# Kernel optimization log

Hardware: AMD Instinct MI355X
Metric: run time of the kernel (lower is better)

## Reference

```python
import jax, jax.numpy as jnp
import numpy as np

B, S, D = 2, 2048, 2048
H = 16
Q_LORA, KV_LORA = 1536, 512
D_NOPE, D_ROPE, D_V = 128, 64, 128
D_QK = D_NOPE + D_ROPE  # 192
EPS = 1e-6


def rmsnorm(x, w):
    return x * jax.lax.rsqrt(jnp.mean(x * x, axis=-1, keepdims=True) + EPS) * w


def apply_rope(x, freqs_cis):
    # x: (B, S, h, D_ROPE); freqs_cis: (S, D_ROPE//2, 2) = (cos, sin)
    # DeepSeek pairs consecutive elements (2i, 2i+1) as complex re/im.
    b, s, h, d = x.shape
    xp = x.reshape(b, s, h, d // 2, 2)
    re, im = xp[..., 0], xp[..., 1]
    cos = freqs_cis[None, :, None, :, 0]
    sin = freqs_cis[None, :, None, :, 1]
    out_re = re * cos - im * sin
    out_im = re * sin + im * cos
    return jnp.stack([out_re, out_im], axis=-1).reshape(b, s, h, d)


def setup_inputs() -> dict:
    key = jax.random.key(0)
    ks = jax.random.split(key, 8)
    sd = 0.02
    x = jax.random.normal(ks[0], (B, S, D), dtype=jnp.float32)
    # RoPE table over the rope head dim
    inv_freq = 1.0 / (10000.0 ** (np.arange(0, D_ROPE, 2, dtype=np.float32) / D_ROPE))
    t = np.arange(S, dtype=np.float32)
    f = np.outer(t, inv_freq)  # (S, 32)
    freqs_cis = jnp.asarray(np.stack([np.cos(f), np.sin(f)], axis=-1), dtype=jnp.float32)
    return {
        "x": x,
        "start_pos": 0,
        "freqs_cis": freqs_cis,
        "wq_a": jax.random.normal(ks[1], (Q_LORA, D), dtype=jnp.float32) * sd,
        "q_norm_w": jnp.ones((Q_LORA,), dtype=jnp.float32),
        "wq_b": jax.random.normal(ks[2], (H * D_QK, Q_LORA), dtype=jnp.float32) * sd,
        "wkv_a": jax.random.normal(ks[3], (KV_LORA + D_ROPE, D), dtype=jnp.float32) * sd,
        "kv_norm_w": jnp.ones((KV_LORA,), dtype=jnp.float32),
        "wkv_b": jax.random.normal(ks[4], (H * (D_NOPE + D_V), KV_LORA), dtype=jnp.float32) * sd,
        "wo": jax.random.normal(ks[5], (D, H * D_V), dtype=jnp.float32) * sd,
    }


def reference(x, start_pos, freqs_cis, wq_a, q_norm_w, wq_b, wkv_a, kv_norm_w, wkv_b, wo):
    bsz, seqlen, _ = x.shape
    softmax_scale = D_QK ** (-0.5)

    # --- queries: low-rank down-proj, RMSNorm, up-proj ---
    q = rmsnorm(x @ wq_a.T, q_norm_w) @ wq_b.T          # (B,S,H*D_QK)
    q = q.reshape(bsz, seqlen, H, D_QK)
    q_nope, q_pe = q[..., :D_NOPE], q[..., D_NOPE:]
    q_pe = apply_rope(q_pe, freqs_cis)
    q = jnp.concatenate([q_nope, q_pe], axis=-1)         # (B,S,H,192)

    # --- keys/values: compressed latent + shared rope key ---
    kv = x @ wkv_a.T                                     # (B,S,KV_LORA+D_ROPE)
    kv_c, k_pe = kv[..., :KV_LORA], kv[..., KV_LORA:]
    k_pe = apply_rope(k_pe[:, :, None, :], freqs_cis)    # (B,S,1,64)
    kvb = rmsnorm(kv_c, kv_norm_w) @ wkv_b.T             # (B,S,H*(D_NOPE+D_V))
    kvb = kvb.reshape(bsz, seqlen, H, D_NOPE + D_V)
    k_nope, v = kvb[..., :D_NOPE], kvb[..., D_NOPE:]
    k = jnp.concatenate([k_nope, jnp.broadcast_to(k_pe, (bsz, seqlen, H, D_ROPE))], axis=-1)

    # --- causal attention (FA2 with attention_mask=None) ---
    scores = jnp.einsum("bqhd,bkhd->bhqk", q, k) * softmax_scale
    causal = jnp.tril(jnp.ones((seqlen, seqlen), dtype=bool))
    scores = jnp.where(causal[None, None], scores, jnp.finfo(scores.dtype).min)
    attn = jax.nn.softmax(scores, axis=-1)
    out = jnp.einsum("bhqk,bkhd->bqhd", attn, v)         # (B,S,H,D_V)
    # (v padding to qk_head_dim then slicing [..., :D_V] is a no-op)
    return out.reshape(bsz, seqlen, H * D_V) @ wo.T
```

## Files before the change

kernel.cpp:

```cpp
#include <hip/hip_runtime.h>
#include <math.h>

typedef short short8 __attribute__((ext_vector_type(8)));
typedef float float4v __attribute__((ext_vector_type(4)));
#define AS1 __attribute__((address_space(1)))
#define AS3 __attribute__((address_space(3)))

__device__ __forceinline__ float b2f(ushort u) {
    unsigned v = ((unsigned)u) << 16; float f; __builtin_memcpy(&f, &v, 4); return f;
}
__device__ __forceinline__ ushort f2b(float f) {
    unsigned v; __builtin_memcpy(&v, &f, 4);
    unsigned r = (v + 0x7fffu + ((v >> 16) & 1u)) >> 16;
    return (ushort)r;
}

__global__ void cvt_pad(const float* __restrict__ src, ushort* __restrict__ dst,
                        int src_rows, int cols, int total4) {
    int i = blockIdx.x * 256 + threadIdx.x;
    if (i >= total4) return;
    size_t e = (size_t)i * 4;
    int r = (int)(e / (size_t)cols);
    ushort4 o;
    if (r < src_rows) {
        float4 v = *(const float4*)(src + e);
        o.x = f2b(v.x); o.y = f2b(v.y); o.z = f2b(v.z); o.w = f2b(v.w);
    } else {
        o.x = 0; o.y = 0; o.z = 0; o.w = 0;
    }
    *(ushort4*)(dst + e) = o;
}

__global__ __launch_bounds__(256)
void gemm_bt(const ushort* __restrict__ A, const ushort* __restrict__ B,
             void* __restrict__ Cv, int K, int ldc, int nstore, int f32out) {
    __shared__ ushort sA[128 * 32];
    __shared__ ushort sB[128 * 32];
    const int tid = threadIdx.x;
    const int wave = tid >> 6, lane = tid & 63;
    const int bm = blockIdx.y * 128, bn = blockIdx.x * 128;
    const int wm = (wave >> 1) * 64, wn = (wave & 1) * 64;
    float4v acc[4][4] = {};

    const int srow = wave * 32 + (lane >> 2);
    const int skc = (lane & 3) * 8;
    const ushort* Ag = A + (size_t)(bm + srow) * K + skc;
    const ushort* Bg = B + (size_t)(bn + srow) * K + skc;
    ushort* sAw = sA + (wave * 32) * 32;
    ushort* sBw = sB + (wave * 32) * 32;

    for (int k0 = 0; k0 < K; k0 += 32) {
        __builtin_amdgcn_global_load_lds((const AS1 void*)(Ag + k0), (AS3 void*)sAw, 16, 0, 0);
        __builtin_amdgcn_global_load_lds((const AS1 void*)(Ag + (size_t)16 * K + k0),
                                         (AS3 void*)(sAw + 16 * 32), 16, 0, 0);
        __builtin_amdgcn_global_load_lds((const AS1 void*)(Bg + k0), (AS3 void*)sBw, 16, 0, 0);
        __builtin_amdgcn_global_load_lds((const AS1 void*)(Bg + (size_t)16 * K + k0),
                                         (AS3 void*)(sBw + 16 * 32), 16, 0, 0);
        __syncthreads();
        short8 af[4], bfr[4];
#pragma unroll
        for (int i = 0; i < 4; ++i) {
            af[i]  = *(const short8*)(sA + (wm + i * 16 + (lane & 15)) * 32 + (lane >> 4) * 8);
            bfr[i] = *(const short8*)(sB + (wn + i * 16 + (lane & 15)) * 32 + (lane >> 4) * 8);
        }
#pragma unroll
        for (int i = 0; i < 4; ++i)
#pragma unroll
            for (int j = 0; j < 4; ++j)
                acc[i][j] = __builtin_amdgcn_mfma_f32_16x16x32_bf16(af[i], bfr[j], acc[i][j], 0, 0, 0);
        __syncthreads();
    }
#pragma unroll
    for (int i = 0; i < 4; ++i) {
        int row0 = bm + wm + i * 16 + (lane >> 4) * 4;
#pragma unroll
        for (int j = 0; j < 4; ++j) {
            int col = bn + wn + j * 16 + (lane & 15);
            if (col < nstore) {
                if (f32out) {
                    float* C = (float*)Cv;
#pragma unroll
                    for (int r = 0; r < 4; ++r)
                        C[(size_t)(row0 + r) * ldc + col] = acc[i][j][r];
                } else {
                    ushort* C = (ushort*)Cv;
#pragma unroll
                    for (int r = 0; r < 4; ++r)
                        C[(size_t)(row0 + r) * ldc + col] = f2b(acc[i][j][r]);
                }
            }
        }
    }
}

__global__ void rmsnorm_inplace(ushort* __restrict__ d, const float* __restrict__ w, int cols) {
    int row = blockIdx.x, tid = threadIdx.x;
    ushort* p = d + (size_t)row * cols;
    float ss = 0.f;
    for (int i = tid; i < cols; i += 256) { float v = b2f(p[i]); ss += v * v; }
#pragma unroll
    for (int off = 32; off >= 1; off >>= 1) ss += __shfl_xor(ss, off);
    __shared__ float red[4];
    if ((tid & 63) == 0) red[tid >> 6] = ss;
    __syncthreads();
    float tot = red[0] + red[1] + red[2] + red[3];
    float rs = rsqrtf(tot / (float)cols + 1e-6f);
    for (int i = tid; i < cols; i += 256) p[i] = f2b(b2f(p[i]) * rs * w[i]);
}

__global__ void kvnorm_rope(const ushort* __restrict__ kvraw, const float* __restrict__ w,
                            const float* __restrict__ freqs, ushort* __restrict__ kvc,
                            ushort* __restrict__ kpe) {
    int row = blockIdx.x, tid = threadIdx.x;
    int s = row & 2047;
    const ushort* p = kvraw + (size_t)row * 576;
    float v0 = b2f(p[tid]), v1 = b2f(p[tid + 256]);
    float ss = v0 * v0 + v1 * v1;
#pragma unroll
    for (int off = 32; off >= 1; off >>= 1) ss += __shfl_xor(ss, off);
    __shared__ float red[4];
    if ((tid & 63) == 0) red[tid >> 6] = ss;
    __syncthreads();
    float tot = red[0] + red[1] + red[2] + red[3];
    float rs = rsqrtf(tot / 512.f + 1e-6f);
    kvc[(size_t)row * 512 + tid] = f2b(v0 * rs * w[tid]);
    kvc[(size_t)row * 512 + tid + 256] = f2b(v1 * rs * w[tid + 256]);
    if (tid < 32) {
        float re = b2f(p[512 + 2 * tid]), im = b2f(p[512 + 2 * tid + 1]);
        float cs = freqs[(s * 32 + tid) * 2], sn = freqs[(s * 32 + tid) * 2 + 1];
        kpe[(size_t)row * 64 + 2 * tid] = f2b(re * cs - im * sn);
        kpe[(size_t)row * 64 + 2 * tid + 1] = f2b(re * sn + im * cs);
    }
}

__global__ void qrope(ushort* __restrict__ q, const float* __restrict__ freqs) {
    int idx = blockIdx.x * 256 + threadIdx.x;
    int i = idx & 31;
    int h = (idx >> 5) & 15;
    int srow = idx >> 9;
    int s = srow & 2047;
    ushort* p = q + ((size_t)srow * 16 + h) * 192 + 128 + 2 * i;
    float re = b2f(p[0]), im = b2f(p[1]);
    float cs = freqs[(s * 32 + i) * 2], sn = freqs[(s * 32 + i) * 2 + 1];
    p[0] = f2b(re * cs - im * sn);
    p[1] = f2b(re * sn + im * cs);
}

__global__ void k_repack(const ushort* __restrict__ kvb, const ushort* __restrict__ kpe,
                         ushort* __restrict__ Kfull) {
    int tid = threadIdx.x;
    int row = blockIdx.x * 8 + (tid >> 5);
    int c = tid & 31;
    int bh = row >> 11, s = row & 2047;
    int b = bh >> 4, h = bh & 15;
    size_t sg = (size_t)b * 2048 + s;
    short8 v = {0, 0, 0, 0, 0, 0, 0, 0};
    if (c < 16)      v = *(const short8*)(kvb + sg * 4096 + h * 256 + c * 8);
    else if (c < 24) v = *(const short8*)(kpe + sg * 64 + (c - 16) * 8);
    if (c < 25) *(short8*)(Kfull + (size_t)row * 200 + c * 8) = v;
}

__global__ __launch_bounds__(256)
void v_repack(const ushort* __restrict__ kvb, ushort* __restrict__ Vt) {
    __shared__ ushort sT[64][136];
    int tid = threadIdx.x;
    int kt = blockIdx.x, bh = blockIdx.y;
    int b = bh >> 4, h = bh & 15;
#pragma unroll
    for (int k = 0; k < 4; ++k) {
        int id = k * 256 + tid;
        int r = id >> 4, c8 = id & 15;
        size_t sg = (size_t)b * 2048 + kt * 64 + r;
        *(short8*)(&sT[r][c8 * 8]) = *(const short8*)(kvb + sg * 4096 + h * 256 + 128 + c8 * 8);
    }
    __syncthreads();
    int d = tid >> 1, half = tid & 1;
    ushort tmp[32];
#pragma unroll
    for (int i = 0; i < 32; ++i) tmp[i] = sT[half * 32 + i][d];
    ushort* dst = Vt + (((size_t)bh * 32 + kt) * 128 + d) * 72 + half * 32;
#pragma unroll
    for (int i = 0; i < 4; ++i) *(short8*)(dst + i * 8) = *(const short8*)(tmp + i * 8);
}

__global__ __launch_bounds__(256)
void mla_attn2(const ushort* __restrict__ q, const ushort* __restrict__ Kfull,
               const ushort* __restrict__ Vt, ushort* __restrict__ out, float scale) {
    __shared__ ushort sK[64 * 200];
    __shared__ ushort sV[128 * 72];
    __shared__ ushort sP[4][16][72];
    const int tid = threadIdx.x, wave = tid >> 6, lane = tid & 63;
    const int p = blockIdx.x, bh = blockIdx.y;
    const int b = bh >> 4, h = bh & 15;
    const ushort* Kb = Kfull + (size_t)bh * 2048 * 200;
    const ushort* Vb = Vt + (size_t)bh * 32 * 128 * 72;

    for (int phase = 0; phase < 2; ++phase) {
        const int qt = (phase == 0) ? (31 - p) : p;
        const int qrow = qt * 64 + wave * 16 + (lane & 15);
        const ushort* qp = q + ((size_t)(b * 2048 + qrow) * 16 + h) * 192 + (lane >> 4) * 8;
        short8 qf[6];
#pragma unroll
        for (int c = 0; c < 6; ++c) qf[c] = *(const short8*)(qp + c * 32);

        float4v oacc[8] = {};
        float m_i[4] = {-INFINITY, -INFINITY, -INFINITY, -INFINITY};
        float l_i[4] = {0.f, 0.f, 0.f, 0.f};
        const int myrow0 = qt * 64 + wave * 16 + (lane >> 4) * 4;

        for (int kt = 0; kt <= qt; ++kt) {
            const ushort* Ksrc = Kb + (size_t)kt * 64 * 200;
            const ushort* Vsrc = Vb + (size_t)kt * 128 * 72;
#pragma unroll
            for (int i = 0; i < 7; ++i) {
                int s0 = i * 256 + wave * 64;
                if (s0 < 1600)
                    __builtin_amdgcn_global_load_lds(
                        (const AS1 void*)(Ksrc + (size_t)(s0 + lane) * 8),
                        (AS3 void*)(sK + s0 * 8), 16, 0, 0);
            }
#pragma unroll
            for (int i = 0; i < 5; ++i) {
                int s0 = i * 256 + wave * 64;
                if (s0 < 1152)
                    __builtin_amdgcn_global_load_lds(
                        (const AS1 void*)(Vsrc + (size_t)(s0 + lane) * 8),
                        (AS3 void*)(sV + s0 * 8), 16, 0, 0);
            }
            __syncthreads();
            float4v sc[4];
#pragma unroll
            for (int ct = 0; ct < 4; ++ct) {
                float4v a = {0.f, 0.f, 0.f, 0.f};
#pragma unroll
                for (int c = 0; c < 6; ++c) {
                    short8 kf = *(const short8*)(sK + (ct * 16 + (lane & 15)) * 200 + c * 32 + (lane >> 4) * 8);
                    a = __builtin_amdgcn_mfma_f32_16x16x32_bf16(qf[c], kf, a, 0, 0, 0);
                }
                sc[ct] = a;
            }
            float mnew[4];
#pragma unroll
            for (int r = 0; r < 4; ++r) mnew[r] = m_i[r];
#pragma unroll
            for (int ct = 0; ct < 4; ++ct)
#pragma unroll
                for (int r = 0; r < 4; ++r) {
                    float v = sc[ct][r] * scale;
                    if (kt == qt && (kt * 64 + ct * 16 + (lane & 15)) > (myrow0 + r)) v = -INFINITY;
                    sc[ct][r] = v;
                    mnew[r] = fmaxf(mnew[r], v);
                }
#pragma unroll
            for (int off = 8; off >= 1; off >>= 1)
#pragma unroll
                for (int r = 0; r < 4; ++r) mnew[r] = fmaxf(mnew[r], __shfl_xor(mnew[r], off));
            float alpha[4], psum[4];
#pragma unroll
            for (int r = 0; r < 4; ++r) {
                alpha[r] = __expf(m_i[r] - mnew[r]);
                m_i[r] = mnew[r];
                psum[r] = 0.f;
            }
#pragma unroll
            for (int ct = 0; ct < 4; ++ct)
#pragma unroll
                for (int r = 0; r < 4; ++r) {
                    float pv = __expf(sc[ct][r] - mnew[r]);
                    psum[r] += pv;
                    sP[wave][(lane >> 4) * 4 + r][ct * 16 + (lane & 15)] = f2b(pv);
                }
#pragma unroll
            for (int off = 8; off >= 1; off >>= 1)
#pragma unroll
                for (int r = 0; r < 4; ++r) psum[r] += __shfl_xor(psum[r], off);
#pragma unroll
            for (int r = 0; r < 4; ++r) l_i[r] = l_i[r] * alpha[r] + psum[r];
#pragma unroll
            for (int dt = 0; dt < 8; ++dt)
#pragma unroll
                for (int r = 0; r < 4; ++r) oacc[dt][r] *= alpha[r];
            __syncthreads();
#pragma unroll
            for (int kc = 0; kc < 2; ++kc) {
                short8 pf = *(const short8*)(&sP[wave][lane & 15][kc * 32 + (lane >> 4) * 8]);
#pragma unroll
                for (int dt = 0; dt < 8; ++dt) {
                    short8 vf = *(const short8*)(sV + (dt * 16 + (lane & 15)) * 72 + kc * 32 + (lane >> 4) * 8);
                    oacc[dt] = __builtin_amdgcn_mfma_f32_16x16x32_bf16(pf, vf, oacc[dt], 0, 0, 0);
                }
            }
            __syncthreads();
        }
#pragma unroll
        for (int dt = 0; dt < 8; ++dt) {
#pragma unroll
            for (int r = 0; r < 4; ++r) {
                int row = myrow0 + r;
                out[((size_t)(b * 2048 + row) * 16 + h) * 128 + dt * 16 + (lane & 15)] =
                    f2b(oacc[dt][r] / l_i[r]);
            }
        }
    }
}

extern "C" void kernel_launch(void* const* d_in, const int* in_sizes, int n_in,
                              void* d_out, int out_size, void* d_ws, size_t ws_size,
                              hipStream_t stream) {
    const float* x     = (const float*)d_in[0];
    const float* freqs = (const float*)d_in[2];
    const float* wq_a  = (const float*)d_in[3];
    const float* qnw   = (const float*)d_in[4];
    const float* wq_b  = (const float*)d_in[5];
    const float* wkv_a = (const float*)d_in[6];
    const float* kvnw  = (const float*)d_in[7];
    const float* wkv_b = (const float*)d_in[8];
    const float* wo    = (const float*)d_in[9];

    char* ws = (char*)d_ws;
    size_t off = 0;
    auto alloc = [&](size_t n) { char* p = ws + off; off += (n + 255) & ~(size_t)255; return p; };
    ushort* xb    = (ushort*)alloc(4096ull * 2048 * 2);
    ushort* wqab  = (ushort*)alloc(1536ull * 2048 * 2);
    ushort* wqbb  = (ushort*)alloc(3072ull * 1536 * 2);
    ushort* wkvab = (ushort*)alloc(640ull * 2048 * 2);
    ushort* wkvbb = (ushort*)alloc(4096ull * 512 * 2);
    ushort* wob   = (ushort*)alloc(2048ull * 2048 * 2);
    ushort* qa    = (ushort*)alloc(4096ull * 1536 * 2);
    ushort* kvraw = (ushort*)alloc(4096ull * 576 * 2);
    ushort* kvc   = (ushort*)alloc(4096ull * 512 * 2);
    ushort* kpe   = (ushort*)alloc(4096ull * 64 * 2);
    ushort* qfull = (ushort*)alloc(4096ull * 3072 * 2);
    ushort* kvbuf = (ushort*)alloc(4096ull * 4096 * 2);
    ushort* attno = (ushort*)alloc(4096ull * 2048 * 2);
    if (off > ws_size) return;
    ushort* Kfull = (ushort*)xb;
    ushort* Vt = (ushort*)qa;

    auto cvt = [&](const float* s, ushort* dd, int sr, int cols, size_t dtot) {
        int t4 = (int)(dtot / 4);
        cvt_pad<<<(t4 + 255) / 256, 256, 0, stream>>>(s, dd, sr, cols, t4);
    };
    cvt(x, xb, 4096, 2048, 4096ull * 2048);
    cvt(wq_a, wqab, 1536, 2048, 1536ull * 2048);
    cvt(wq_b, wqbb, 3072, 1536, 3072ull * 1536);
    cvt(wkv_a, wkvab, 576, 2048, 640ull * 2048);
    cvt(wkv_b, wkvbb, 4096, 512, 4096ull * 512);
    cvt(wo, wob, 2048, 2048, 2048ull * 2048);

    gemm_bt<<<dim3(12, 32), 256, 0, stream>>>(xb, wqab, qa, 2048, 1536, 1536, 0);
    gemm_bt<<<dim3(5, 32), 256, 0, stream>>>(xb, wkvab, kvraw, 2048, 576, 576, 0);
    rmsnorm_inplace<<<4096, 256, 0, stream>>>(qa, qnw, 1536);
    kvnorm_rope<<<4096, 256, 0, stream>>>(kvraw, kvnw, freqs, kvc, kpe);
    gemm_bt<<<dim3(24, 32), 256, 0, stream>>>(qa, wqbb, qfull, 1536, 3072, 3072, 0);
    qrope<<<8192, 256, 0, stream>>>(qfull, freqs);
    gemm_bt<<<dim3(32, 32), 256, 0, stream>>>(kvc, wkvbb, kvbuf, 512, 4096, 4096, 0);
    k_repack<<<8192, 256, 0, stream>>>(kvbuf, kpe, Kfull);
    v_repack<<<dim3(32, 32), 256, 0, stream>>>(kvbuf, Vt);
    const float scale = 1.0f / sqrtf(192.0f);
    mla_attn2<<<dim3(16, 32), 256, 0, stream>>>(qfull, Kfull, Vt, attno, scale);
    gemm_bt<<<dim3(16, 32), 256, 0, stream>>>(attno, wob, (float*)d_out, 2048, 2048, 2048, 1);
}
```

Before: 550.2 us.

## Fuse q/kv down-projection GEMMs and rework attention to keep P in registers

The two down-projection weight matrices are packed into one buffer, so a single GEMM produces the q latent and the kv latent into a shared strided buffer. The norm and GEMM kernels gain leading-dimension arguments to read from it. The attention kernel now computes S^T (K as the A operand), so each lane owns one query row. This lets softmax stats reduce across only two shuffles and P feed the PV MFMA straight from registers, removing the LDS round trip and a barrier. The grid changes from 16 paired-phase blocks to 32 single-tile blocks, and the PV product uses 16x16x16 MFMAs, which issue more, smaller instructions.

```diff
diff --git a/kernel.cpp b/kernel.cpp
--- a/kernel.cpp
+++ b/kernel.cpp
@@ -2,6 +2,7 @@
 #include <math.h>
 
 typedef short short8 __attribute__((ext_vector_type(8)));
+typedef short short4v __attribute__((ext_vector_type(4)));
 typedef float float4v __attribute__((ext_vector_type(4)));
 #define AS1 __attribute__((address_space(1)))
 #define AS3 __attribute__((address_space(3)))
@@ -13,6 +14,18 @@
     unsigned v; __builtin_memcpy(&v, &f, 4);
     unsigned r = (v + 0x7fffu + ((v >> 16) & 1u)) >> 16;
     return (ushort)r;
+}
+
+__device__ __forceinline__ float4v pv_mfma(short4v a, short4v b, float4v c) {
+#if __has_builtin(__builtin_amdgcn_mfma_f32_16x16x16_bf16)
+    return __builtin_amdgcn_mfma_f32_16x16x16_bf16(a, b, c, 0, 0, 0);
+#elif __has_builtin(__builtin_amdgcn_mfma_f32_16x16x16bf16_1k)
+    return __builtin_amdgcn_mfma_f32_16x16x16bf16_1k(a, b, c, 0, 0, 0);
+#else
+    short8 a8 = {a[0], a[1], a[2], a[3], 0, 0, 0, 0};
+    short8 b8 = {b[0], b[1], b[2], b[3], 0, 0, 0, 0};
+    return __builtin_amdgcn_mfma_f32_16x16x32_bf16(a8, b8, c, 0, 0, 0);
+#endif
 }
 
 __global__ void cvt_pad(const float* __restrict__ src, ushort* __restrict__ dst,
@@ -33,7 +46,7 @@
 
 __global__ __launch_bounds__(256)
 void gemm_bt(const ushort* __restrict__ A, const ushort* __restrict__ B,
-             void* __restrict__ Cv, int K, int ldc, int nstore, int f32out) {
+             void* __restrict__ Cv, int K, int lda, int ldb, int ldc, int f32out) {
     __shared__ ushort sA[128 * 32];
     __shared__ ushort sB[128 * 32];
     const int tid = threadIdx.x;
@@ -44,17 +57,17 @@
 
     const int srow = wave * 32 + (lane >> 2);
     const int skc = (lane & 3) * 8;
-    const ushort* Ag = A + (size_t)(bm + srow) * K + skc;
-    const ushort* Bg = B + (size_t)(bn + srow) * K + skc;
+    const ushort* Ag = A + (size_t)(bm + srow) * lda + skc;
+    const ushort* Bg = B + (size_t)(bn + srow) * ldb + skc;
     ushort* sAw = sA + (wave * 32) * 32;
     ushort* sBw = sB + (wave * 32) * 32;
 
     for (int k0 = 0; k0 < K; k0 += 32) {
         __builtin_amdgcn_global_load_lds((const AS1 void*)(Ag + k0), (AS3 void*)sAw, 16, 0, 0);
-        __builtin_amdgcn_global_load_lds((const AS1 void*)(Ag + (size_t)16 * K + k0),
+        __builtin_amdgcn_global_load_lds((const AS1 void*)(Ag + (size_t)16 * lda + k0),
                                          (AS3 void*)(sAw + 16 * 32), 16, 0, 0);
         __builtin_amdgcn_global_load_lds((const AS1 void*)(Bg + k0), (AS3 void*)sBw, 16, 0, 0);
-        __builtin_amdgcn_global_load_lds((const AS1 void*)(Bg + (size_t)16 * K + k0),
+        __builtin_amdgcn_global_load_lds((const AS1 void*)(Bg + (size_t)16 * ldb + k0),
                                          (AS3 void*)(sBw + 16 * 32), 16, 0, 0);
         __syncthreads();
         short8 af[4], bfr[4];
@@ -76,26 +89,25 @@
 #pragma unroll
         for (int j = 0; j < 4; ++j) {
             int col = bn + wn + j * 16 + (lane & 15);
-            if (col < nstore) {
-                if (f32out) {
-                    float* C = (float*)Cv;
-#pragma unroll
-                    for (int r = 0; r < 4; ++r)
-                        C[(size_t)(row0 + r) * ldc + col] = acc[i][j][r];
-                } else {
-                    ushort* C = (ushort*)Cv;
-#pragma unroll
-                    for (int r = 0; r < 4; ++r)
-                        C[(size_t)(row0 + r) * ldc + col] = f2b(acc[i][j][r]);
-                }
-            }
-        }
-    }
-}
-
-__global__ void rmsnorm_inplace(ushort* __restrict__ d, const float* __restrict__ w, int cols) {
+            if (f32out) {
+                float* C = (float*)Cv;
+#pragma unroll
+                for (int r = 0; r < 4; ++r)
+                    C[(size_t)(row0 + r) * ldc + col] = acc[i][j][r];
+            } else {
+                ushort* C = (ushort*)Cv;
+#pragma unroll
+                for (int r = 0; r < 4; ++r)
+                    C[(size_t)(row0 + r) * ldc + col] = f2b(acc[i][j][r]);
+            }
+        }
+    }
+}
+
+__global__ void rmsnorm_inplace(ushort* __restrict__ d, const float* __restrict__ w,
+                                int cols, int ld) {
     int row = blockIdx.x, tid = threadIdx.x;
-    ushort* p = d + (size_t)row * cols;
+    ushort* p = d + (size_t)row * ld;
     float ss = 0.f;
     for (int i = tid; i < cols; i += 256) { float v = b2f(p[i]); ss += v * v; }
 #pragma unroll
@@ -110,10 +122,10 @@
 
 __global__ void kvnorm_rope(const ushort* __restrict__ kvraw, const float* __restrict__ w,
                             const float* __restrict__ freqs, ushort* __restrict__ kvc,
-                            ushort* __restrict__ kpe) {
+                            ushort* __restrict__ kpe, int ld) {
     int row = blockIdx.x, tid = threadIdx.x;
     int s = row & 2047;
-    const ushort* p = kvraw + (size_t)row * 576;
+    const ushort* p = kvraw + (size_t)row * ld;
     float v0 = b2f(p[tid]), v1 = b2f(p[tid + 256]);
     float ss = v0 * v0 + v1 * v1;
 #pragma unroll
@@ -184,123 +196,106 @@
 }
 
 __global__ __launch_bounds__(256)
-void mla_attn2(const ushort* __restrict__ q, const ushort* __restrict__ Kfull,
+void mla_attn3(const ushort* __restrict__ q, const ushort* __restrict__ Kfull,
                const ushort* __restrict__ Vt, ushort* __restrict__ out, float scale) {
     __shared__ ushort sK[64 * 200];
     __shared__ ushort sV[128 * 72];
-    __shared__ ushort sP[4][16][72];
     const int tid = threadIdx.x, wave = tid >> 6, lane = tid & 63;
-    const int p = blockIdx.x, bh = blockIdx.y;
+    const int lq = lane & 15, quad = lane >> 4;
+    const int qt = 31 - blockIdx.x;
+    const int bh = blockIdx.y;
     const int b = bh >> 4, h = bh & 15;
     const ushort* Kb = Kfull + (size_t)bh * 2048 * 200;
     const ushort* Vb = Vt + (size_t)bh * 32 * 128 * 72;
 
-    for (int phase = 0; phase < 2; ++phase) {
-        const int qt = (phase == 0) ? (31 - p) : p;
-        const int qrow = qt * 64 + wave * 16 + (lane & 15);
-        const ushort* qp = q + ((size_t)(b * 2048 + qrow) * 16 + h) * 192 + (lane >> 4) * 8;
-        short8 qf[6];
-#pragma unroll
-        for (int c = 0; c < 6; ++c) qf[c] = *(const short8*)(qp + c * 32);
-
-        float4v oacc[8] = {};
-        float m_i[4] = {-INFINITY, -INFINITY, -INFINITY, -INFINITY};
-        float l_i[4] = {0.f, 0.f, 0.f, 0.f};
-        const int myrow0 = qt * 64 + wave * 16 + (lane >> 4) * 4;
-
-        for (int kt = 0; kt <= qt; ++kt) {
-            const ushort* Ksrc = Kb + (size_t)kt * 64 * 200;
-            const ushort* Vsrc = Vb + (size_t)kt * 128 * 72;
-#pragma unroll
-            for (int i = 0; i < 7; ++i) {
-                int s0 = i * 256 + wave * 64;
-                if (s0 < 1600)
-                    __builtin_amdgcn_global_load_lds(
-                        (const AS1 void*)(Ksrc + (size_t)(s0 + lane) * 8),
-                        (AS3 void*)(sK + s0 * 8), 16, 0, 0);
-            }
-#pragma unroll
-            for (int i = 0; i < 5; ++i) {
-                int s0 = i * 256 + wave * 64;
-                if (s0 < 1152)
-                    __builtin_amdgcn_global_load_lds(
-                        (const AS1 void*)(Vsrc + (size_t)(s0 + lane) * 8),
-                        (AS3 void*)(sV + s0 * 8), 16, 0, 0);
-            }
-            __syncthreads();
-            float4v sc[4];
+    const int q_abs = qt * 64 + wave * 16 + lq;
+    const ushort* qp = q + ((size_t)(b * 2048 + q_abs) * 16 + h) * 192 + quad * 8;
+    short8 qf[6];
+#pragma unroll
+    for (int c = 0; c < 6; ++c) qf[c] = *(const short8*)(qp + c * 32);
+
+    float4v oacc[8] = {};
+    float m_i = -INFINITY, l_i = 0.f;
+
+    for (int kt = 0; kt <= qt; ++kt) {
+        const ushort* Ksrc = Kb + (size_t)kt * 64 * 200;
+        const ushort* Vsrc = Vb + (size_t)kt * 128 * 72;
+#pragma unroll
+        for (int i = 0; i < 7; ++i) {
+            int s0 = i * 256 + wave * 64;
+            if (s0 < 1600)
+                __builtin_amdgcn_global_load_lds((const AS1 void*)(Ksrc + (size_t)(s0 + lane) * 8),
+                                                 (AS3 void*)(sK + s0 * 8), 16, 0, 0);
+        }
+#pragma unroll
+        for (int i = 0; i < 5; ++i) {
+            int s0 = i * 256 + wave * 64;
+            if (s0 < 1152)
+                __builtin_amdgcn_global_load_lds((const AS1 void*)(Vsrc + (size_t)(s0 + lane) * 8),
+                                                 (AS3 void*)(sV + s0 * 8), 16, 0, 0);
+        }
+        __syncthreads();
+        float4v sc[4];
+#pragma unroll
+        for (int ct = 0; ct < 4; ++ct) {
+            float4v a = {0.f, 0.f, 0.f, 0.f};
+#pragma unroll
+            for (int c = 0; c < 6; ++c) {
+                short8 kf = *(const short8*)(sK + (ct * 16 + lq) * 200 + c * 32 + quad * 8);
+                a = __builtin_amdgcn_mfma_f32_16x16x32_bf16(kf, qf[c], a, 0, 0, 0);
+            }
+            sc[ct] = a;
+        }
+        float mx = m_i;
+#pragma unroll
+        for (int ct = 0; ct < 4; ++ct)
+#pragma unroll
+            for (int r = 0; r < 4; ++r) {
+                float v = sc[ct][r] * scale;
+                int kv = kt * 64 + ct * 16 + quad * 4 + r;
+                if (kv > q_abs) v = -INFINITY;
+                sc[ct][r] = v;
+                mx = fmaxf(mx, v);
+            }
+        mx = fmaxf(mx, __shfl_xor(mx, 16));
+        mx = fmaxf(mx, __shfl_xor(mx, 32));
+        float alpha = __expf(m_i - mx);
+        m_i = mx;
+        float ps = 0.f;
+        short4v pf[4];
+#pragma unroll
+        for (int ct = 0; ct < 4; ++ct)
+#pragma unroll
+            for (int r = 0; r < 4; ++r) {
+                float pv = __expf(sc[ct][r] - mx);
+                ps += pv;
+                pf[ct][r] = (short)f2b(pv);
+            }
+        ps += __shfl_xor(ps, 16);
+        ps += __shfl_xor(ps, 32);
+        l_i = l_i * alpha + ps;
+#pragma unroll
+        for (int dt = 0; dt < 8; ++dt)
+#pragma unroll
+            for (int r = 0; r < 4; ++r) oacc[dt][r] *= alpha;
+#pragma unroll
+        for (int dt = 0; dt < 8; ++dt)
 #pragma unroll
             for (int ct = 0; ct < 4; ++ct) {
-                float4v a = {0.f, 0.f, 0.f, 0.f};
-#pragma unroll
-                for (int c = 0; c < 6; ++c) {
-                    short8 kf = *(const short8*)(sK + (ct * 16 + (lane & 15)) * 200 + c * 32 + (lane >> 4) * 8);
-                    a = __builtin_amdgcn_mfma_f32_16x16x32_bf16(qf[c], kf, a, 0, 0, 0);
-                }
-                sc[ct] = a;
-            }
-            float mnew[4];
-#pragma unroll
-            for (int r = 0; r < 4; ++r) mnew[r] = m_i[r];
-#pragma unroll
-            for (int ct = 0; ct < 4; ++ct)
-#pragma unroll
-                for (int r = 0; r < 4; ++r) {
-                    float v = sc[ct][r] * scale;
-                    if (kt == qt && (kt * 64 + ct * 16 + (lane & 15)) > (myrow0 + r)) v = -INFINITY;
-                    sc[ct][r] = v;
-                    mnew[r] = fmaxf(mnew[r], v);
-                }
-#pragma unroll
-            for (int off = 8; off >= 1; off >>= 1)
-#pragma unroll
-                for (int r = 0; r < 4; ++r) mnew[r] = fmaxf(mnew[r], __shfl_xor(mnew[r], off));
-            float alpha[4], psum[4];
-#pragma unroll
-            for (int r = 0; r < 4; ++r) {
-                alpha[r] = __expf(m_i[r] - mnew[r]);
-                m_i[r] = mnew[r];
-                psum[r] = 0.f;
-            }
-#pragma unroll
-            for (int ct = 0; ct < 4; ++ct)
-#pragma unroll
-                for (int r = 0; r < 4; ++r) {
-                    float pv = __expf(sc[ct][r] - mnew[r]);
-                    psum[r] += pv;
-                    sP[wave][(lane >> 4) * 4 + r][ct * 16 + (lane & 15)] = f2b(pv);
-                }
-#pragma unroll
-            for (int off = 8; off >= 1; off >>= 1)
-#pragma unroll
-                for (int r = 0; r < 4; ++r) psum[r] += __shfl_xor(psum[r], off);
-#pragma unroll
-            for (int r = 0; r < 4; ++r) l_i[r] = l_i[r] * alpha[r] + psum[r];
-#pragma unroll
-            for (int dt = 0; dt < 8; ++dt)
-#pragma unroll
-                for (int r = 0; r < 4; ++r) oacc[dt][r] *= alpha[r];
-            __syncthreads();
-#pragma unroll
-            for (int kc = 0; kc < 2; ++kc) {
-                short8 pf = *(const short8*)(&sP[wave][lane & 15][kc * 32 + (lane >> 4) * 8]);
-#pragma unroll
-                for (int dt = 0; dt < 8; ++dt) {
-                    short8 vf = *(const short8*)(sV + (dt * 16 + (lane & 15)) * 72 + kc * 32 + (lane >> 4) * 8);
-                    oacc[dt] = __builtin_amdgcn_mfma_f32_16x16x32_bf16(pf, vf, oacc[dt], 0, 0, 0);
-                }
-            }
-            __syncthreads();
-        }
-#pragma unroll
-        for (int dt = 0; dt < 8; ++dt) {
-#pragma unroll
-            for (int r = 0; r < 4; ++r) {
-                int row = myrow0 + r;
-                out[((size_t)(b * 2048 + row) * 16 + h) * 128 + dt * 16 + (lane & 15)] =
-                    f2b(oacc[dt][r] / l_i[r]);
-            }
-        }
+                short4v vf = *(const short4v*)(sV + (dt * 16 + lq) * 72 + ct * 16 + quad * 4);
+                oacc[dt] = pv_mfma(vf, pf[ct], oacc[dt]);
+            }
+        __syncthreads();
+    }
+    float inv = 1.f / l_i;
+#pragma unroll
+    for (int dt = 0; dt < 8; ++dt) {
+        ushort4 o;
+        o.x = f2b(oacc[dt][0] * inv);
+        o.y = f2b(oacc[dt][1] * inv);
+        o.z = f2b(oacc[dt][2] * inv);
+        o.w = f2b(oacc[dt][3] * inv);
+        *(ushort4*)(out + ((size_t)(b * 2048 + q_abs) * 16 + h) * 128 + dt * 16 + quad * 4) = o;
     }
 }
 
@@ -321,13 +316,11 @@
     size_t off = 0;
     auto alloc = [&](size_t n) { char* p = ws + off; off += (n + 255) & ~(size_t)255; return p; };
     ushort* xb    = (ushort*)alloc(4096ull * 2048 * 2);
-    ushort* wqab  = (ushort*)alloc(1536ull * 2048 * 2);
+    ushort* wqkva = (ushort*)alloc(2176ull * 2048 * 2);
     ushort* wqbb  = (ushort*)alloc(3072ull * 1536 * 2);
-    ushort* wkvab = (ushort*)alloc(640ull * 2048 * 2);
     ushort* wkvbb = (ushort*)alloc(4096ull * 512 * 2);
     ushort* wob   = (ushort*)alloc(2048ull * 2048 * 2);
-    ushort* qa    = (ushort*)alloc(4096ull * 1536 * 2);
-    ushort* kvraw = (ushort*)alloc(4096ull * 576 * 2);
+    ushort* qakv  = (ushort*)alloc(4096ull * 2176 * 2);
     ushort* kvc   = (ushort*)alloc(4096ull * 512 * 2);
     ushort* kpe   = (ushort*)alloc(4096ull * 64 * 2);
     ushort* qfull = (ushort*)alloc(4096ull * 3072 * 2);
@@ -335,29 +328,28 @@
     ushort* attno = (ushort*)alloc(4096ull * 2048 * 2);
     if (off > ws_size) return;
     ushort* Kfull = (ushort*)xb;
-    ushort* Vt = (ushort*)qa;
+    ushort* Vt = (ushort*)qakv;
 
     auto cvt = [&](const float* s, ushort* dd, int sr, int cols, size_t dtot) {
         int t4 = (int)(dtot / 4);
         cvt_pad<<<(t4 + 255) / 256, 256, 0, stream>>>(s, dd, sr, cols, t4);
     };
     cvt(x, xb, 4096, 2048, 4096ull * 2048);
-    cvt(wq_a, wqab, 1536, 2048, 1536ull * 2048);
+    cvt(wq_a, wqkva, 1536, 2048, 1536ull * 2048);
+    cvt(wkv_a, wqkva + 1536ull * 2048, 576, 2048, 640ull * 2048);
     cvt(wq_b, wqbb, 3072, 1536, 3072ull * 1536);
-    cvt(wkv_a, wkvab, 576, 2048, 640ull * 2048);
     cvt(wkv_b, wkvbb, 4096, 512, 4096ull * 512);
     cvt(wo, wob, 2048, 2048, 2048ull * 2048);
 
-    gemm_bt<<<dim3(12, 32), 256, 0, stream>>>(xb, wqab, qa, 2048, 1536, 1536, 0);
-    gemm_bt<<<dim3(5, 32), 256, 0, stream>>>(xb, wkvab, kvraw, 2048, 576, 576, 0);
-    rmsnorm_inplace<<<4096, 256, 0, stream>>>(qa, qnw, 1536);
-    kvnorm_rope<<<4096, 256, 0, stream>>>(kvraw, kvnw, freqs, kvc, kpe);
-    gemm_bt<<<dim3(24, 32), 256, 0, stream>>>(qa, wqbb, qfull, 1536, 3072, 3072, 0);
+    gemm_bt<<<dim3(17, 32), 256, 0, stream>>>(xb, wqkva, qakv, 2048, 2048, 2048, 2176, 0);
+    rmsnorm_inplace<<<4096, 256, 0, stream>>>(qakv, qnw, 1536, 2176);
+    kvnorm_rope<<<4096, 256, 0, stream>>>(qakv + 1536, kvnw, freqs, kvc, kpe, 2176);
+    gemm_bt<<<dim3(24, 32), 256, 0, stream>>>(qakv, wqbb, qfull, 1536, 2176, 1536, 3072, 0);
     qrope<<<8192, 256, 0, stream>>>(qfull, freqs);
-    gemm_bt<<<dim3(32, 32), 256, 0, stream>>>(kvc, wkvbb, kvbuf, 512, 4096, 4096, 0);
+    gemm_bt<<<dim3(32, 32), 256, 0, stream>>>(kvc, wkvbb, kvbuf, 512, 512, 512, 4096, 0);
     k_repack<<<8192, 256, 0, stream>>>(kvbuf, kpe, Kfull);
     v_repack<<<dim3(32, 32), 256, 0, stream>>>(kvbuf, Vt);
     const float scale = 1.0f / sqrtf(192.0f);
-    mla_attn2<<<dim3(16, 32), 256, 0, stream>>>(qfull, Kfull, Vt, attno, scale);
-    gemm_bt<<<dim3(16, 32), 256, 0, stream>>>(attno, wob, (float*)d_out, 2048, 2048, 2048, 1);
-}
+    mla_attn3<<<dim3(32, 32), 256, 0, stream>>>(qfull, Kfull, Vt, attno, scale);
+    gemm_bt<<<dim3(16, 32), 256, 0, stream>>>(attno, wob, (float*)d_out, 2048, 2048, 2048, 2048, 1);
+}
```

After: 561.3 us. 2.0% more time.

## Merge q/kv down-projections and fuse K/V repacking into up-projection epilogue

Applied to the files above, without the earlier changes.

The q and kv down-projection weights are concatenated so a single GEMM computes both, and the norm kernels read them through a row stride. The kv up-projection GEMM gains a scatter epilogue that writes K-nope straight into the padded K layout and V transposed into the attention tile layout, which removes the k_repack and v_repack kernels and the intermediate kvbuf round trip. A small kernel fills the rope part of K. The attention kernel also drops one barrier before the PV step, since each wave only reads its own P slice, and replaces the per-element divide with a multiply by a reciprocal. The V epilogue writes scattered 8-byte stores, which may coalesce poorly.

```diff
diff --git a/kernel.cpp b/kernel.cpp
--- a/kernel.cpp
+++ b/kernel.cpp
@@ -33,35 +33,37 @@
 
 __global__ __launch_bounds__(256)
 void gemm_bt(const ushort* __restrict__ A, const ushort* __restrict__ B,
-             void* __restrict__ Cv, int K, int ldc, int nstore, int f32out) {
+             void* __restrict__ Cv, int K, int lda, int ldb, int ldc, int mode,
+             ushort* __restrict__ Kf, ushort* __restrict__ Vtp) {
     __shared__ ushort sA[128 * 32];
     __shared__ ushort sB[128 * 32];
     const int tid = threadIdx.x;
     const int wave = tid >> 6, lane = tid & 63;
     const int bm = blockIdx.y * 128, bn = blockIdx.x * 128;
     const int wm = (wave >> 1) * 64, wn = (wave & 1) * 64;
+    const int lq = lane & 15, quad = lane >> 4;
     float4v acc[4][4] = {};
 
     const int srow = wave * 32 + (lane >> 2);
     const int skc = (lane & 3) * 8;
-    const ushort* Ag = A + (size_t)(bm + srow) * K + skc;
-    const ushort* Bg = B + (size_t)(bn + srow) * K + skc;
+    const ushort* Ag = A + (size_t)(bm + srow) * lda + skc;
+    const ushort* Bg = B + (size_t)(bn + srow) * ldb + skc;
     ushort* sAw = sA + (wave * 32) * 32;
     ushort* sBw = sB + (wave * 32) * 32;
 
     for (int k0 = 0; k0 < K; k0 += 32) {
         __builtin_amdgcn_global_load_lds((const AS1 void*)(Ag + k0), (AS3 void*)sAw, 16, 0, 0);
-        __builtin_amdgcn_global_load_lds((const AS1 void*)(Ag + (size_t)16 * K + k0),
+        __builtin_amdgcn_global_load_lds((const AS1 void*)(Ag + (size_t)16 * lda + k0),
                                          (AS3 void*)(sAw + 16 * 32), 16, 0, 0);
         __builtin_amdgcn_global_load_lds((const AS1 void*)(Bg + k0), (AS3 void*)sBw, 16, 0, 0);
-        __builtin_amdgcn_global_load_lds((const AS1 void*)(Bg + (size_t)16 * K + k0),
+        __builtin_amdgcn_global_load_lds((const AS1 void*)(Bg + (size_t)16 * ldb + k0),
                                          (AS3 void*)(sBw + 16 * 32), 16, 0, 0);
         __syncthreads();
         short8 af[4], bfr[4];
 #pragma unroll
         for (int i = 0; i < 4; ++i) {
-            af[i]  = *(const short8*)(sA + (wm + i * 16 + (lane & 15)) * 32 + (lane >> 4) * 8);
-            bfr[i] = *(const short8*)(sB + (wn + i * 16 + (lane & 15)) * 32 + (lane >> 4) * 8);
+            af[i]  = *(const short8*)(sA + (wm + i * 16 + lq) * 32 + quad * 8);
+            bfr[i] = *(const short8*)(sB + (wn + i * 16 + lq) * 32 + quad * 8);
         }
 #pragma unroll
         for (int i = 0; i < 4; ++i)
@@ -72,30 +74,46 @@
     }
 #pragma unroll
     for (int i = 0; i < 4; ++i) {
-        int row0 = bm + wm + i * 16 + (lane >> 4) * 4;
+        int row0 = bm + wm + i * 16 + quad * 4;
 #pragma unroll
         for (int j = 0; j < 4; ++j) {
-            int col = bn + wn + j * 16 + (lane & 15);
-            if (col < nstore) {
-                if (f32out) {
-                    float* C = (float*)Cv;
-#pragma unroll
-                    for (int r = 0; r < 4; ++r)
-                        C[(size_t)(row0 + r) * ldc + col] = acc[i][j][r];
+            int col = bn + wn + j * 16 + lq;
+            if (mode == 0) {
+                ushort* C = (ushort*)Cv;
+#pragma unroll
+                for (int r = 0; r < 4; ++r)
+                    C[(size_t)(row0 + r) * ldc + col] = f2b(acc[i][j][r]);
+            } else if (mode == 1) {
+                float* C = (float*)Cv;
+#pragma unroll
+                for (int r = 0; r < 4; ++r)
+                    C[(size_t)(row0 + r) * ldc + col] = acc[i][j][r];
+            } else {
+                int h = col >> 8, c = col & 255;
+                int bh = ((row0 >> 11) << 4) + h;
+                if (c < 128) {
+#pragma unroll
+                    for (int r = 0; r < 4; ++r) {
+                        int s = (row0 + r) & 2047;
+                        Kf[((size_t)bh * 2048 + s) * 200 + c] = f2b(acc[i][j][r]);
+                    }
                 } else {
-                    ushort* C = (ushort*)Cv;
-#pragma unroll
-                    for (int r = 0; r < 4; ++r)
-                        C[(size_t)(row0 + r) * ldc + col] = f2b(acc[i][j][r]);
+                    int d = c - 128;
+                    int kt = (row0 & 2047) >> 6, kv = row0 & 63;
+                    ushort4 o;
+                    o.x = f2b(acc[i][j][0]); o.y = f2b(acc[i][j][1]);
+                    o.z = f2b(acc[i][j][2]); o.w = f2b(acc[i][j][3]);
+                    *(ushort4*)(Vtp + (((size_t)bh * 32 + kt) * 128 + d) * 72 + kv) = o;
                 }
             }
         }
     }
 }
 
-__global__ void rmsnorm_inplace(ushort* __restrict__ d, const float* __restrict__ w, int cols) {
+__global__ void rmsnorm_inplace(ushort* __restrict__ d, const float* __restrict__ w,
+                                int cols, int ld) {
     int row = blockIdx.x, tid = threadIdx.x;
-    ushort* p = d + (size_t)row * cols;
+    ushort* p = d + (size_t)row * ld;
     float ss = 0.f;
     for (int i = tid; i < cols; i += 256) { float v = b2f(p[i]); ss += v * v; }
 #pragma unroll
@@ -110,10 +128,10 @@
 
 __global__ void kvnorm_rope(const ushort* __restrict__ kvraw, const float* __restrict__ w,
                             const float* __restrict__ freqs, ushort* __restrict__ kvc,
-                            ushort* __restrict__ kpe) {
+                            ushort* __restrict__ kpe, int ld) {
     int row = blockIdx.x, tid = threadIdx.x;
     int s = row & 2047;
-    const ushort* p = kvraw + (size_t)row * 576;
+    const ushort* p = kvraw + (size_t)row * ld;
     float v0 = b2f(p[tid]), v1 = b2f(p[tid + 256]);
     float ss = v0 * v0 + v1 * v1;
 #pragma unroll
@@ -146,50 +164,25 @@
     p[1] = f2b(re * sn + im * cs);
 }
 
-__global__ void k_repack(const ushort* __restrict__ kvb, const ushort* __restrict__ kpe,
-                         ushort* __restrict__ Kfull) {
+__global__ void kpe_fill(const ushort* __restrict__ kpe, ushort* __restrict__ Kfull) {
     int tid = threadIdx.x;
     int row = blockIdx.x * 8 + (tid >> 5);
     int c = tid & 31;
-    int bh = row >> 11, s = row & 2047;
-    int b = bh >> 4, h = bh & 15;
-    size_t sg = (size_t)b * 2048 + s;
-    short8 v = {0, 0, 0, 0, 0, 0, 0, 0};
-    if (c < 16)      v = *(const short8*)(kvb + sg * 4096 + h * 256 + c * 8);
-    else if (c < 24) v = *(const short8*)(kpe + sg * 64 + (c - 16) * 8);
-    if (c < 25) *(short8*)(Kfull + (size_t)row * 200 + c * 8) = v;
+    int bh = row >> 11, s = row & 2047, b = bh >> 4;
+    ushort2 v;
+    v.x = kpe[((size_t)b * 2048 + s) * 64 + 2 * c];
+    v.y = kpe[((size_t)b * 2048 + s) * 64 + 2 * c + 1];
+    *(ushort2*)(Kfull + (size_t)row * 200 + 128 + 2 * c) = v;
 }
 
 __global__ __launch_bounds__(256)
-void v_repack(const ushort* __restrict__ kvb, ushort* __restrict__ Vt) {
-    __shared__ ushort sT[64][136];
-    int tid = threadIdx.x;
-    int kt = blockIdx.x, bh = blockIdx.y;
-    int b = bh >> 4, h = bh & 15;
-#pragma unroll
-    for (int k = 0; k < 4; ++k) {
-        int id = k * 256 + tid;
-        int r = id >> 4, c8 = id & 15;
-        size_t sg = (size_t)b * 2048 + kt * 64 + r;
-        *(short8*)(&sT[r][c8 * 8]) = *(const short8*)(kvb + sg * 4096 + h * 256 + 128 + c8 * 8);
-    }
-    __syncthreads();
-    int d = tid >> 1, half = tid & 1;
-    ushort tmp[32];
-#pragma unroll
-    for (int i = 0; i < 32; ++i) tmp[i] = sT[half * 32 + i][d];
-    ushort* dst = Vt + (((size_t)bh * 32 + kt) * 128 + d) * 72 + half * 32;
-#pragma unroll
-    for (int i = 0; i < 4; ++i) *(short8*)(dst + i * 8) = *(const short8*)(tmp + i * 8);
-}
-
-__global__ __launch_bounds__(256)
-void mla_attn2(const ushort* __restrict__ q, const ushort* __restrict__ Kfull,
+void mla_attn5(const ushort* __restrict__ q, const ushort* __restrict__ Kfull,
                const ushort* __restrict__ Vt, ushort* __restrict__ out, float scale) {
     __shared__ ushort sK[64 * 200];
     __shared__ ushort sV[128 * 72];
     __shared__ ushort sP[4][16][72];
     const int tid = threadIdx.x, wave = tid >> 6, lane = tid & 63;
+    const int lq = lane & 15, quad = lane >> 4;
     const int p = blockIdx.x, bh = blockIdx.y;
     const int b = bh >> 4, h = bh & 15;
     const ushort* Kb = Kfull + (size_t)bh * 2048 * 200;
@@ -197,8 +190,8 @@
 
     for (int phase = 0; phase < 2; ++phase) {
         const int qt = (phase == 0) ? (31 - p) : p;
-        const int qrow = qt * 64 + wave * 16 + (lane & 15);
-        const ushort* qp = q + ((size_t)(b * 2048 + qrow) * 16 + h) * 192 + (lane >> 4) * 8;
+        const int qrow = qt * 64 + wave * 16 + lq;
+        const ushort* qp = q + ((size_t)(b * 2048 + qrow) * 16 + h) * 192 + quad * 8;
         short8 qf[6];
 #pragma unroll
         for (int c = 0; c < 6; ++c) qf[c] = *(const short8*)(qp + c * 32);
@@ -206,7 +199,7 @@
         float4v oacc[8] = {};
         float m_i[4] = {-INFINITY, -INFINITY, -INFINITY, -INFINITY};
         float l_i[4] = {0.f, 0.f, 0.f, 0.f};
-        const int myrow0 = qt * 64 + wave * 16 + (lane >> 4) * 4;
+        const int myrow0 = qt * 64 + wave * 16 + quad * 4;
 
         for (int kt = 0; kt <= qt; ++kt) {
             const ushort* Ksrc = Kb + (size_t)kt * 64 * 200;
@@ -215,17 +208,15 @@
             for (int i = 0; i < 7; ++i) {
                 int s0 = i * 256 + wave * 64;
                 if (s0 < 1600)
-                    __builtin_amdgcn_global_load_lds(
-                        (const AS1 void*)(Ksrc + (size_t)(s0 + lane) * 8),
-                        (AS3 void*)(sK + s0 * 8), 16, 0, 0);
+                    __builtin_amdgcn_global_load_lds((const AS1 void*)(Ksrc + (size_t)(s0 + lane) * 8),
+                                                     (AS3 void*)(sK + s0 * 8), 16, 0, 0);
             }
 #pragma unroll
             for (int i = 0; i < 5; ++i) {
                 int s0 = i * 256 + wave * 64;
                 if (s0 < 1152)
-                    __builtin_amdgcn_global_load_lds(
-                        (const AS1 void*)(Vsrc + (size_t)(s0 + lane) * 8),
-                        (AS3 void*)(sV + s0 * 8), 16, 0, 0);
+                    __builtin_amdgcn_global_load_lds((const AS1 void*)(Vsrc + (size_t)(s0 + lane) * 8),
+                                                     (AS3 void*)(sV + s0 * 8), 16, 0, 0);
             }
             __syncthreads();
             float4v sc[4];
@@ -234,7 +225,7 @@
                 float4v a = {0.f, 0.f, 0.f, 0.f};
 #pragma unroll
                 for (int c = 0; c < 6; ++c) {
-                    short8 kf = *(const short8*)(sK + (ct * 16 + (lane & 15)) * 200 + c * 32 + (lane >> 4) * 8);
+                    short8 kf = *(const short8*)(sK + (ct * 16 + lq) * 200 + c * 32 + quad * 8);
                     a = __builtin_amdgcn_mfma_f32_16x16x32_bf16(qf[c], kf, a, 0, 0, 0);
                 }
                 sc[ct] = a;
@@ -247,7 +238,7 @@
 #pragma unroll
                 for (int r = 0; r < 4; ++r) {
                     float v = sc[ct][r] * scale;
-                    if (kt == qt && (kt * 64 + ct * 16 + (lane & 15)) > (myrow0 + r)) v = -INFINITY;
+                    if (kt == qt && (kt * 64 + ct * 16 + lq) > (myrow0 + r)) v = -INFINITY;
                     sc[ct][r] = v;
                     mnew[r] = fmaxf(mnew[r], v);
                 }
@@ -268,7 +259,7 @@
                 for (int r = 0; r < 4; ++r) {
                     float pv = __expf(sc[ct][r] - mnew[r]);
                     psum[r] += pv;
-                    sP[wave][(lane >> 4) * 4 + r][ct * 16 + (lane & 15)] = f2b(pv);
+                    sP[wave][quad * 4 + r][ct * 16 + lq] = f2b(pv);
                 }
 #pragma unroll
             for (int off = 8; off >= 1; off >>= 1)
@@ -280,25 +271,26 @@
             for (int dt = 0; dt < 8; ++dt)
 #pragma unroll
                 for (int r = 0; r < 4; ++r) oacc[dt][r] *= alpha[r];
-            __syncthreads();
 #pragma unroll
             for (int kc = 0; kc < 2; ++kc) {
-                short8 pf = *(const short8*)(&sP[wave][lane & 15][kc * 32 + (lane >> 4) * 8]);
+                short8 pf = *(const short8*)(&sP[wave][lq][kc * 32 + quad * 8]);
 #pragma unroll
                 for (int dt = 0; dt < 8; ++dt) {
-                    short8 vf = *(const short8*)(sV + (dt * 16 + (lane & 15)) * 72 + kc * 32 + (lane >> 4) * 8);
+                    short8 vf = *(const short8*)(sV + (dt * 16 + lq) * 72 + kc * 32 + quad * 8);
                     oacc[dt] = __builtin_amdgcn_mfma_f32_16x16x32_bf16(pf, vf, oacc[dt], 0, 0, 0);
                 }
             }
             __syncthreads();
         }
+        float inv[4];
+#pragma unroll
+        for (int r = 0; r < 4; ++r) inv[r] = 1.f / l_i[r];
 #pragma unroll
         for (int dt = 0; dt < 8; ++dt) {
 #pragma unroll
             for (int r = 0; r < 4; ++r) {
-                int row = myrow0 + r;
-                out[((size_t)(b * 2048 + row) * 16 + h) * 128 + dt * 16 + (lane & 15)] =
-                    f2b(oacc[dt][r] / l_i[r]);
+                out[((size_t)(b * 2048 + myrow0 + r) * 16 + h) * 128 + dt * 16 + lq] =
+                    f2b(oacc[dt][r] * inv[r]);
             }
         }
     }
@@ -321,43 +313,39 @@
     size_t off = 0;
     auto alloc = [&](size_t n) { char* p = ws + off; off += (n + 255) & ~(size_t)255; return p; };
     ushort* xb    = (ushort*)alloc(4096ull * 2048 * 2);
-    ushort* wqab  = (ushort*)alloc(1536ull * 2048 * 2);
+    ushort* wqkva = (ushort*)alloc(2176ull * 2048 * 2);
     ushort* wqbb  = (ushort*)alloc(3072ull * 1536 * 2);
-    ushort* wkvab = (ushort*)alloc(640ull * 2048 * 2);
     ushort* wkvbb = (ushort*)alloc(4096ull * 512 * 2);
     ushort* wob   = (ushort*)alloc(2048ull * 2048 * 2);
-    ushort* qa    = (ushort*)alloc(4096ull * 1536 * 2);
-    ushort* kvraw = (ushort*)alloc(4096ull * 576 * 2);
+    ushort* qakv  = (ushort*)alloc(4096ull * 2176 * 2);
     ushort* kvc   = (ushort*)alloc(4096ull * 512 * 2);
     ushort* kpe   = (ushort*)alloc(4096ull * 64 * 2);
     ushort* qfull = (ushort*)alloc(4096ull * 3072 * 2);
     ushort* kvbuf = (ushort*)alloc(4096ull * 4096 * 2);
     ushort* attno = (ushort*)alloc(4096ull * 2048 * 2);
     if (off > ws_size) return;
-    ushort* Kfull = (ushort*)xb;
-    ushort* Vt = (ushort*)qa;
+    ushort* Kfull = kvbuf;
+    ushort* Vt = xb;
 
     auto cvt = [&](const float* s, ushort* dd, int sr, int cols, size_t dtot) {
         int t4 = (int)(dtot / 4);
         cvt_pad<<<(t4 + 255) / 256, 256, 0, stream>>>(s, dd, sr, cols, t4);
     };
     cvt(x, xb, 4096, 2048, 4096ull * 2048);
-    cvt(wq_a, wqab, 1536, 2048, 1536ull * 2048);
+    cvt(wq_a, wqkva, 1536, 2048, 1536ull * 2048);
+    cvt(wkv_a, wqkva + 1536ull * 2048, 576, 2048, 640ull * 2048);
     cvt(wq_b, wqbb, 3072, 1536, 3072ull * 1536);
-    cvt(wkv_a, wkvab, 576, 2048, 640ull * 2048);
     cvt(wkv_b, wkvbb, 4096, 512, 4096ull * 512);
     cvt(wo, wob, 2048, 2048, 2048ull * 2048);
 
-    gemm_bt<<<dim3(12, 32), 256, 0, stream>>>(xb, wqab, qa, 2048, 1536, 1536, 0);
-    gemm_bt<<<dim3(5, 32), 256, 0, stream>>>(xb, wkvab, kvraw, 2048, 576, 576, 0);
-    rmsnorm_inplace<<<4096, 256, 0, stream>>>(qa, qnw, 1536);
-    kvnorm_rope<<<4096, 256, 0, stream>>>(kvraw, kvnw, freqs, kvc, kpe);
-    gemm_bt<<<dim3(24, 32), 256, 0, stream>>>(qa, wqbb, qfull, 1536, 3072, 3072, 0);
+    gemm_bt<<<dim3(17, 32), 256, 0, stream>>>(xb, wqkva, qakv, 2048, 2048, 2048, 2176, 0, nullptr, nullptr);
+    rmsnorm_inplace<<<4096, 256, 0, stream>>>(qakv, qnw, 1536, 2176);
+    kvnorm_rope<<<4096, 256, 0, stream>>>(qakv + 1536, kvnw, freqs, kvc, kpe, 2176);
+    gemm_bt<<<dim3(24, 32), 256, 0, stream>>>(qakv, wqbb, qfull, 1536, 2176, 1536, 3072, 0, nullptr, nullptr);
     qrope<<<8192, 256, 0, stream>>>(qfull, freqs);
-    gemm_bt<<<dim3(32, 32), 256, 0, stream>>>(kvc, wkvbb, kvbuf, 512, 4096, 4096, 0);
-    k_repack<<<8192, 256, 0, stream>>>(kvbuf, kpe, Kfull);
-    v_repack<<<dim3(32, 32), 256, 0, stream>>>(kvbuf, Vt);
+    kpe_fill<<<8192, 256, 0, stream>>>(kpe, Kfull);
+    gemm_bt<<<dim3(32, 32), 256, 0, stream>>>(kvc, wkvbb, nullptr, 512, 512, 512, 0, 2, Kfull, Vt);
     const float scale = 1.0f / sqrtf(192.0f);
-    mla_attn2<<<dim3(16, 32), 256, 0, stream>>>(qfull, Kfull, Vt, attno, scale);
-    gemm_bt<<<dim3(16, 32), 256, 0, stream>>>(attno, wob, (float*)d_out, 2048, 2048, 2048, 1);
-}
+    mla_attn5<<<dim3(16, 32), 256, 0, stream>>>(qfull, Kfull, Vt, attno, scale);
+    gemm_bt<<<dim3(16, 32), 256, 0, stream>>>(attno, wob, (float*)d_out, 2048, 2048, 2048, 2048, 1, nullptr, nullptr);
+}
```

Result: faster. 509.2 us (-7.5%).
